# Performance work log

Measured on AMD Instinct MI355X. Metric: run time of the kernel, lower is better.

## Reference

```python
import jax, jax.numpy as jnp
import numpy as np

B, T, N = 8, 4096, 1024
N_KNOWN = 768  # known (sampled) nodes; unknown = N - N_KNOWN = 256
DENSITY = 0.03


def setup_inputs() -> dict:
    key = jax.random.key(0)
    k1, k2, k3, k4 = jax.random.split(key, 4)
    x = jax.random.normal(k1, (B, T, N), dtype=jnp.float32)
    # binary adjacency with ~DENSITY edges; add identity so every node has >=1 neighbor
    A = (jax.random.uniform(k2, (N, N)) < DENSITY).astype(jnp.float32)
    A = jnp.maximum(A, jnp.eye(N, dtype=jnp.float32))
    # unknown = complement(sample, N): 256 distinct node ids, ascending (set-iteration order)
    perm = jax.random.permutation(k3, N)
    unknown = jnp.sort(perm[N_KNOWN:]).astype(jnp.int32)
    # mask = scalar mean of matrix.values[:, sample] in the original module
    mask = jax.random.uniform(k4, (), dtype=jnp.float32)
    return {"input": x, "A": A, "unknown": unknown, "mask": mask}


def reference(input, A, unknown, mask):
    # 1) overwrite unknown columns with the scalar mask (in-place in the original)
    x = input.at[:, :, unknown].set(mask)
    deg = jnp.sum(A, axis=1)  # [N] neighbor counts (A is binary)
    # 2) sequential in-place per-node neighbor mean: later unknown nodes see
    #    the already-updated values of earlier ones, so order matters -> lax.scan.
    def step(x, node):
        # mean over neighbors == masked weighted sum via the binary adjacency row
        val = jnp.einsum('btn,n->bt', x, A[node]) / deg[node]  # [B, T]
        return x.at[:, :, node].set(val), None
    x, _ = jax.lax.scan(step, x, unknown)
    return x
```

## Files before the change

kernel.cpp:

```cpp
#include <hip/hip_runtime.h>

#define U 256
#define NN 1024
#define NROWS 32768
#define LCAP 32
#define DUMMY 256

typedef __bf16 bf16_t;
typedef __bf16 bf16x4 __attribute__((ext_vector_type(4)));
typedef __bf16 bf16x8 __attribute__((ext_vector_type(8)));
typedef float f32x4 __attribute__((ext_vector_type(4)));
typedef unsigned short u16;
typedef unsigned short u16x8 __attribute__((ext_vector_type(8)));
typedef short s16x4 __attribute__((ext_vector_type(4)));

__global__ __launch_bounds__(256) void k_struct(const float* __restrict__ A,
    const int* __restrict__ unknown, const float* __restrict__ maskp,
    float* __restrict__ invDeg, float* __restrict__ coef,
    int* __restrict__ lessCnt, u16* __restrict__ lessIdx,
    int* __restrict__ uflag, short* __restrict__ pmap)
{
    __shared__ int sunk[U];
    __shared__ float sdeg;
    __shared__ int scnt, sge;
    int t = threadIdx.x, k = blockIdx.x;
    sunk[t] = unknown[t];
    if (t == 0) { sdeg = 0.f; scnt = 0; sge = 0; }
    __syncthreads();
    int uk = sunk[k];
    float dsum = 0.f;
    for (int i = 0; i < NN / 256; ++i) {
        int n = t + 256 * i;
        float a = A[(size_t)uk * NN + n];
        if (a != 0.f) {
            dsum += a;
            int lo = 0, hi = U;
            while (lo < hi) { int mid = (lo + hi) >> 1; if (sunk[mid] < n) lo = mid + 1; else hi = mid; }
            if (lo < U && sunk[lo] == n) {
                if (lo < k) {
                    int id = atomicAdd(&scnt, 1);
                    if (id < LCAP) lessIdx[k * LCAP + id] = (u16)lo;
                } else {
                    atomicAdd(&sge, 1);
                }
            }
        }
    }
    atomicAdd(&sdeg, dsum);
    __syncthreads();
    int c0 = min(scnt, LCAP);
    if (t >= c0 && t < LCAP) lessIdx[k * LCAP + t] = DUMMY;
    if (t == 0) {
        float inv = 1.f / sdeg;
        invDeg[k] = inv;
        coef[k] = (float)sge * maskp[0] * inv;
        lessCnt[k] = c0;
    }
    if (k == 0) {
        for (int i = 0; i < NN / 256; ++i) { uflag[t + 256 * i] = 0; pmap[t + 256 * i] = -1; }
        __syncthreads();
        uflag[sunk[t]] = 1;
        pmap[sunk[t]] = (short)t;
    }
}

__global__ __launch_bounds__(256) void k_levels(const int* __restrict__ lessCnt,
    const u16* __restrict__ lessIdx, int* __restrict__ order,
    int* __restrict__ levelStart, int* __restrict__ nLevOut)
{
    __shared__ u16 sIdx[U * LCAP];
    __shared__ int slvl[U];
    __shared__ int sc[U];
    __shared__ int hist[U];
    __shared__ int changed;
    int t = threadIdx.x;
    for (int i = t; i < U * LCAP / 2; i += 256) ((unsigned int*)sIdx)[i] = ((const unsigned int*)lessIdx)[i];
    sc[t] = lessCnt[t];
    slvl[t] = 0; hist[t] = 0;
    __syncthreads();
    for (int iter = 0; iter < U; ++iter) {
        if (t == 0) changed = 0;
        __syncthreads();
        int c = sc[t], nl = 0;
        for (int i = 0; i < c; ++i) nl = max(nl, slvl[sIdx[t * LCAP + i]] + 1);
        if (nl > slvl[t]) { slvl[t] = nl; changed = 1; }
        __syncthreads();
        if (!changed) break;
    }
    int L = slvl[t];
    atomicAdd(&hist[L], 1);
    __syncthreads();
    if (t == 0) {
        int acc = 0, lastl = 0;
        for (int l = 0; l < U; ++l) {
            int h = hist[l];
            hist[l] = acc;
            acc += h;
            if (h > 0) lastl = l;
        }
        nLevOut[0] = lastl + 1;
    }
    __syncthreads();
    levelStart[t] = hist[t];
    if (t == 0) levelStart[U] = U;
    __syncthreads();
    int pos = atomicAdd(&hist[L], 1);
    order[pos] = t;
}

__global__ __launch_bounds__(256) void k_mbuild(const int* __restrict__ lessCnt,
    const u16* __restrict__ lessIdx, const float* __restrict__ invDeg,
    const int* __restrict__ order, const int* __restrict__ levelStart,
    const int* __restrict__ nLevp, float* __restrict__ MT)
{
    __shared__ float Ms[(U + 1) * 32];
    __shared__ u16 sIdx[U * LCAP];
    __shared__ float sInv[U];
    __shared__ u16 sOrd[U];
    __shared__ unsigned char sCnt[U];
    __shared__ int sLs[U + 1];
    int t = threadIdx.x;
    int g = t >> 5, c = t & 31;
    int col = blockIdx.x * 32 + c;
    for (int i = t; i < U * LCAP / 2; i += 256) ((unsigned int*)sIdx)[i] = ((const unsigned int*)lessIdx)[i];
    sInv[t] = invDeg[t];
    sOrd[t] = (u16)order[t];
    sCnt[t] = (unsigned char)lessCnt[t];
    sLs[t] = levelStart[t];
    if (t == 0) sLs[U] = levelStart[U];
    if (t < 32) Ms[U * 32 + t] = 0.f;
    int nLev = nLevp[0];
    __syncthreads();
    for (int lev = 0; lev < nLev; ++lev) {
        int s = sLs[lev], e = sLs[lev + 1];
        for (int base = s + g; base < e; base += 8) {
            int k = sOrd[base];
            int cnt = sCnt[k];
            const u16* ip = &sIdx[k * LCAP];
            float sum = 0.f;
            for (int b = 0; b < cnt; b += 8) {
                u16x8 jv = *(const u16x8*)(ip + b);
                float v0 = Ms[jv[0] * 32 + c];
                float v1 = Ms[jv[1] * 32 + c];
                float v2 = Ms[jv[2] * 32 + c];
                float v3 = Ms[jv[3] * 32 + c];
                float v4 = Ms[jv[4] * 32 + c];
                float v5 = Ms[jv[5] * 32 + c];
                float v6 = Ms[jv[6] * 32 + c];
                float v7 = Ms[jv[7] * 32 + c];
                sum += ((v0 + v1) + (v2 + v3)) + ((v4 + v5) + (v6 + v7));
            }
            float m = (k == col ? 1.f : 0.f) + sInv[k] * sum;
            Ms[k * 32 + c] = m;
            MT[(size_t)col * U + k] = m;
        }
        __syncthreads();
    }
}

__global__ __launch_bounds__(256) void k_wbuild(const float* __restrict__ A,
    const int* __restrict__ unknown, const float* __restrict__ invDeg,
    const float* __restrict__ coef, const int* __restrict__ uflag,
    const float* __restrict__ MT, bf16_t* __restrict__ Wb, float* __restrict__ bvec)
{
    int t = threadIdx.x, d = blockIdx.x;
    if (d == NN) {
        __shared__ float scf[U];
        scf[t] = coef[t];
        __syncthreads();
        float s = 0.f;
        #pragma unroll 8
        for (int c = 0; c < U; ++c) s += MT[(size_t)c * U + t] * scf[c];
        bvec[t] = s;
        return;
    }
    if (uflag[d]) { Wb[(size_t)t * NN + d] = (bf16_t)0.f; return; }
    __shared__ int nnz;
    __shared__ int cs[64];
    __shared__ float vsv[64];
    if (t == 0) nnz = 0;
    __syncthreads();
    float a = A[(size_t)unknown[t] * NN + d];
    if (a != 0.f) {
        int id = atomicAdd(&nnz, 1);
        if (id < 64) { cs[id] = t; vsv[id] = a * invDeg[t]; }
    }
    __syncthreads();
    int n = min(nnz, 64);
    float s = 0.f;
    for (int i = 0; i < n; ++i)
        s += MT[(size_t)cs[i] * U + t] * vsv[i];
    Wb[(size_t)t * NN + d] = (bf16_t)s;
}

#define RT 32
#define BK 64
#define LDX 72
#define URS 257

__global__ __launch_bounds__(256) void k_main(const float* __restrict__ x,
    const short* __restrict__ pmap, const bf16_t* __restrict__ Wb,
    const float* __restrict__ bvec, float* __restrict__ out)
{
    __shared__ __align__(16) char smem[41472];
    __shared__ float sb[U];
    __shared__ short spm[NN];
    bf16_t* Xl = (bf16_t*)smem;
    bf16_t* Vl = (bf16_t*)(smem + 4608);
    float* Ures = (float*)smem;
    int t = threadIdx.x;
    int w = t >> 6, l = t & 63;
    int m = l & 15, q = l >> 4;
    size_t row0 = (size_t)blockIdx.x * RT;
    sb[t] = bvec[t];
    #pragma unroll
    for (int j = 0; j < 4; ++j) spm[t + 256 * j] = pmap[t + 256 * j];
    f32x4 acc[2][4] = {};
    int uv = t >> 3, du = (t & 7) * 8;
    for (int db = 0; db < NN; db += BK) {
        __syncthreads();
        #pragma unroll
        for (int ii = 0; ii < 2; ++ii) {
            int flat = t + ii * 256;
            int r = flat >> 4, c4 = (flat & 15) * 4;
            float4 v = *(const float4*)(x + (row0 + r) * NN + db + c4);
            bf16x4 hv = { (bf16_t)v.x, (bf16_t)v.y, (bf16_t)v.z, (bf16_t)v.w };
            *(bf16x4*)(&Xl[r * LDX + c4]) = hv;
        }
        #pragma unroll
        for (int i = 0; i < 8; ++i) {
            int u = uv + 32 * i;
            *(bf16x8*)(&Vl[u * LDX + du]) = *(const bf16x8*)(Wb + (size_t)u * NN + db + du);
        }
        __syncthreads();
        #pragma unroll
        for (int s = 0; s < 2; ++s) {
            bf16x8 af[2];
            #pragma unroll
            for (int R = 0; R < 2; ++R)
                af[R] = *(bf16x8*)(&Xl[(R * 16 + m) * LDX + s * 32 + q * 8]);
            #pragma unroll
            for (int T = 0; T < 4; ++T) {
                bf16x8 bfr = *(bf16x8*)(&Vl[((w * 4 + T) * 16 + m) * LDX + s * 32 + q * 8]);
                #pragma unroll
                for (int R = 0; R < 2; ++R)
                    acc[R][T] = __builtin_amdgcn_mfma_f32_16x16x32_bf16(af[R], bfr, acc[R][T], 0, 0, 0);
            }
        }
    }
    __syncthreads();
    #pragma unroll
    for (int R = 0; R < 2; ++R) {
        #pragma unroll
        for (int T = 0; T < 4; ++T) {
            int u = (w * 4 + T) * 16 + m;
            float bb = sb[u];
            #pragma unroll
            for (int i = 0; i < 4; ++i)
                Ures[(R * 16 + q * 4 + i) * URS + u] = acc[R][T][i] + bb;
        }
    }
    __syncthreads();
    s16x4 pm = *(const s16x4*)(&spm[t * 4]);
    #pragma unroll 4
    for (int i = 0; i < RT; ++i) {
        float4 v = *(const float4*)(x + (row0 + i) * NN + t * 4);
        if (pm[0] >= 0) v.x = Ures[i * URS + pm[0]];
        if (pm[1] >= 0) v.y = Ures[i * URS + pm[1]];
        if (pm[2] >= 0) v.z = Ures[i * URS + pm[2]];
        if (pm[3] >= 0) v.w = Ures[i * URS + pm[3]];
        *(float4*)(out + (row0 + i) * NN + t * 4) = v;
    }
}

extern "C" void kernel_launch(void* const* d_in, const int* in_sizes, int n_in,
                              void* d_out, int out_size, void* d_ws, size_t ws_size,
                              hipStream_t stream)
{
    const float* x       = (const float*)d_in[0];
    const float* A       = (const float*)d_in[1];
    const int*   unknown = (const int*)d_in[2];
    const float* maskp   = (const float*)d_in[3];
    float* out = (float*)d_out;

    char* ws = (char*)d_ws;
    float*  MT        = (float*)(ws + 0);
    bf16_t* Wb        = (bf16_t*)(ws + 262144);
    float*  invDeg    = (float*)(ws + 786432);
    float*  coef      = (float*)(ws + 787456);
    float*  bvec      = (float*)(ws + 788480);
    int*    lessCnt   = (int*)(ws + 789504);
    u16*    lessIdx   = (u16*)(ws + 790528);
    int*    uflag     = (int*)(ws + 806912);
    short*  pmap      = (short*)(ws + 811008);
    int*    order     = (int*)(ws + 813056);
    int*    levelStart= (int*)(ws + 814080);
    int*    nLev      = (int*)(ws + 815120);

    hipLaunchKernelGGL(k_struct, dim3(U), dim3(256), 0, stream,
                       A, unknown, maskp, invDeg, coef, lessCnt, lessIdx, uflag, pmap);
    hipLaunchKernelGGL(k_levels, dim3(1), dim3(256), 0, stream,
                       lessCnt, lessIdx, order, levelStart, nLev);
    hipLaunchKernelGGL(k_mbuild, dim3(8), dim3(256), 0, stream,
                       lessCnt, lessIdx, invDeg, order, levelStart, nLev, MT);
    hipLaunchKernelGGL(k_wbuild, dim3(NN + 1), dim3(256), 0, stream,
                       A, unknown, invDeg, coef, uflag, MT, Wb, bvec);
    hipLaunchKernelGGL(k_main, dim3(NROWS / RT), dim3(256), 0, stream,
                       x, pmap, Wb, bvec, out);
}
```

Before: 348.2 us.

## Double the row tile and prefetch next K-chunk into registers

The main GEMM kernel now processes 64 rows per block instead of 32, so each Wb tile loaded into LDS is reused across twice as many rows. Global loads for the next K-chunk are issued into registers before the MFMA work on the current chunk, so load latency overlaps compute. The epilogue writes results in two halves to fit the existing Ures buffer, and launch bounds ask for two blocks per CU. Costs are more registers per thread and half as many blocks (512), which may reduce occupancy and parallelism.

```diff
diff --git a/kernel.cpp b/kernel.cpp
--- a/kernel.cpp
+++ b/kernel.cpp
@@ -193,20 +193,20 @@
     Wb[(size_t)t * NN + d] = (bf16_t)s;
 }
 
-#define RT 32
+#define RT 64
 #define BK 64
 #define LDX 72
 #define URS 257
 
-__global__ __launch_bounds__(256) void k_main(const float* __restrict__ x,
+__global__ __launch_bounds__(256, 2) void k_main(const float* __restrict__ x,
     const short* __restrict__ pmap, const bf16_t* __restrict__ Wb,
     const float* __restrict__ bvec, float* __restrict__ out)
 {
-    __shared__ __align__(16) char smem[41472];
+    __shared__ __align__(16) char smem[46080];
     __shared__ float sb[U];
     __shared__ short spm[NN];
     bf16_t* Xl = (bf16_t*)smem;
-    bf16_t* Vl = (bf16_t*)(smem + 4608);
+    bf16_t* Vl = (bf16_t*)(smem + 9216);
     float* Ures = (float*)smem;
     int t = threadIdx.x;
     int w = t >> 6, l = t & 63;
@@ -215,61 +215,82 @@
     sb[t] = bvec[t];
     #pragma unroll
     for (int j = 0; j < 4; ++j) spm[t + 256 * j] = pmap[t + 256 * j];
-    f32x4 acc[2][4] = {};
+    f32x4 acc[4][4] = {};
     int uv = t >> 3, du = (t & 7) * 8;
+
+    float4 xr[4];
+    bf16x8 vr[8];
+
+#define LOADC(DB) do { \
+    _Pragma("unroll") \
+    for (int ii = 0; ii < 4; ++ii) { \
+        int flat = t + ii * 256; \
+        int r = flat >> 4, c4 = (flat & 15) * 4; \
+        xr[ii] = *(const float4*)(x + (row0 + r) * NN + (DB) + c4); \
+    } \
+    _Pragma("unroll") \
+    for (int i = 0; i < 8; ++i) \
+        vr[i] = *(const bf16x8*)(Wb + (size_t)(uv + 32 * i) * NN + (DB) + du); \
+} while (0)
+
+    LOADC(0);
     for (int db = 0; db < NN; db += BK) {
         __syncthreads();
         #pragma unroll
-        for (int ii = 0; ii < 2; ++ii) {
+        for (int ii = 0; ii < 4; ++ii) {
             int flat = t + ii * 256;
             int r = flat >> 4, c4 = (flat & 15) * 4;
-            float4 v = *(const float4*)(x + (row0 + r) * NN + db + c4);
+            float4 v = xr[ii];
             bf16x4 hv = { (bf16_t)v.x, (bf16_t)v.y, (bf16_t)v.z, (bf16_t)v.w };
             *(bf16x4*)(&Xl[r * LDX + c4]) = hv;
         }
         #pragma unroll
-        for (int i = 0; i < 8; ++i) {
-            int u = uv + 32 * i;
-            *(bf16x8*)(&Vl[u * LDX + du]) = *(const bf16x8*)(Wb + (size_t)u * NN + db + du);
-        }
-        __syncthreads();
+        for (int i = 0; i < 8; ++i)
+            *(bf16x8*)(&Vl[(uv + 32 * i) * LDX + du]) = vr[i];
+        __syncthreads();
+        if (db + BK < NN) LOADC(db + BK);
         #pragma unroll
         for (int s = 0; s < 2; ++s) {
-            bf16x8 af[2];
+            bf16x8 af[4];
             #pragma unroll
-            for (int R = 0; R < 2; ++R)
+            for (int R = 0; R < 4; ++R)
                 af[R] = *(bf16x8*)(&Xl[(R * 16 + m) * LDX + s * 32 + q * 8]);
             #pragma unroll
             for (int T = 0; T < 4; ++T) {
                 bf16x8 bfr = *(bf16x8*)(&Vl[((w * 4 + T) * 16 + m) * LDX + s * 32 + q * 8]);
                 #pragma unroll
-                for (int R = 0; R < 2; ++R)
+                for (int R = 0; R < 4; ++R)
                     acc[R][T] = __builtin_amdgcn_mfma_f32_16x16x32_bf16(af[R], bfr, acc[R][T], 0, 0, 0);
             }
         }
     }
-    __syncthreads();
+#undef LOADC
     #pragma unroll
-    for (int R = 0; R < 2; ++R) {
+    for (int h = 0; h < 2; ++h) {
+        __syncthreads();
         #pragma unroll
-        for (int T = 0; T < 4; ++T) {
-            int u = (w * 4 + T) * 16 + m;
-            float bb = sb[u];
+        for (int R2 = 0; R2 < 2; ++R2) {
+            int R = 2 * h + R2;
             #pragma unroll
-            for (int i = 0; i < 4; ++i)
-                Ures[(R * 16 + q * 4 + i) * URS + u] = acc[R][T][i] + bb;
-        }
-    }
-    __syncthreads();
-    s16x4 pm = *(const s16x4*)(&spm[t * 4]);
-    #pragma unroll 4
-    for (int i = 0; i < RT; ++i) {
-        float4 v = *(const float4*)(x + (row0 + i) * NN + t * 4);
-        if (pm[0] >= 0) v.x = Ures[i * URS + pm[0]];
-        if (pm[1] >= 0) v.y = Ures[i * URS + pm[1]];
-        if (pm[2] >= 0) v.z = Ures[i * URS + pm[2]];
-        if (pm[3] >= 0) v.w = Ures[i * URS + pm[3]];
-        *(float4*)(out + (row0 + i) * NN + t * 4) = v;
+            for (int T = 0; T < 4; ++T) {
+                int u = (w * 4 + T) * 16 + m;
+                float bb = sb[u];
+                #pragma unroll
+                for (int i = 0; i < 4; ++i)
+                    Ures[(R2 * 16 + q * 4 + i) * URS + u] = acc[R][T][i] + bb;
+            }
+        }
+        __syncthreads();
+        s16x4 pm = *(const s16x4*)(&spm[t * 4]);
+        #pragma unroll 4
+        for (int i = 0; i < 32; ++i) {
+            float4 v = *(const float4*)(x + (row0 + h * 32 + i) * NN + t * 4);
+            if (pm[0] >= 0) v.x = Ures[i * URS + pm[0]];
+            if (pm[1] >= 0) v.y = Ures[i * URS + pm[1]];
+            if (pm[2] >= 0) v.z = Ures[i * URS + pm[2]];
+            if (pm[3] >= 0) v.w = Ures[i * URS + pm[3]];
+            *(float4*)(out + (row0 + h * 32 + i) * NN + t * 4) = v;
+        }
     }
 }
 
```

Result: faster. 323.4 us (-7.1%).

## Fuse setup kernels into one cooperative launch and prefetch next tile in main GEMM

Applied to the files above, without the earlier changes.

Merges the four preprocessing kernels (structure, levels, M build, W build) into a single cooperative kernel separated by grid syncs, removing three launch gaps. The W build now has 256 blocks each handling four columns. The main kernel register-prefetches the next x and W tile before the MFMA loop to overlap global loads with compute, and raises launch bounds to target three blocks per CU. The cooperative launch needs all 256 blocks to be co-resident, and the extra prefetch registers may raise register pressure.

```diff
diff --git a/kernel.cpp b/kernel.cpp
--- a/kernel.cpp
+++ b/kernel.cpp
@@ -1,4 +1,7 @@
 #include <hip/hip_runtime.h>
+#include <hip/hip_cooperative_groups.h>
+
+namespace cg = cooperative_groups;
 
 #define U 256
 #define NN 1024
@@ -14,183 +17,193 @@
 typedef unsigned short u16x8 __attribute__((ext_vector_type(8)));
 typedef short s16x4 __attribute__((ext_vector_type(4)));
 
-__global__ __launch_bounds__(256) void k_struct(const float* __restrict__ A,
+__global__ __launch_bounds__(256) void k_setup(const float* __restrict__ A,
     const int* __restrict__ unknown, const float* __restrict__ maskp,
     float* __restrict__ invDeg, float* __restrict__ coef,
     int* __restrict__ lessCnt, u16* __restrict__ lessIdx,
-    int* __restrict__ uflag, short* __restrict__ pmap)
+    int* __restrict__ uflag, short* __restrict__ pmap,
+    int* __restrict__ order, int* __restrict__ levelStart, int* __restrict__ nLev,
+    float* __restrict__ MT, bf16_t* __restrict__ Wb, float* __restrict__ bvec)
 {
+    cg::grid_group grid = cg::this_grid();
     __shared__ int sunk[U];
     __shared__ float sdeg;
     __shared__ int scnt, sge;
-    int t = threadIdx.x, k = blockIdx.x;
-    sunk[t] = unknown[t];
-    if (t == 0) { sdeg = 0.f; scnt = 0; sge = 0; }
-    __syncthreads();
-    int uk = sunk[k];
-    float dsum = 0.f;
-    for (int i = 0; i < NN / 256; ++i) {
-        int n = t + 256 * i;
-        float a = A[(size_t)uk * NN + n];
-        if (a != 0.f) {
-            dsum += a;
-            int lo = 0, hi = U;
-            while (lo < hi) { int mid = (lo + hi) >> 1; if (sunk[mid] < n) lo = mid + 1; else hi = mid; }
-            if (lo < U && sunk[lo] == n) {
-                if (lo < k) {
-                    int id = atomicAdd(&scnt, 1);
-                    if (id < LCAP) lessIdx[k * LCAP + id] = (u16)lo;
-                } else {
-                    atomicAdd(&sge, 1);
-                }
-            }
-        }
-    }
-    atomicAdd(&sdeg, dsum);
-    __syncthreads();
-    int c0 = min(scnt, LCAP);
-    if (t >= c0 && t < LCAP) lessIdx[k * LCAP + t] = DUMMY;
-    if (t == 0) {
-        float inv = 1.f / sdeg;
-        invDeg[k] = inv;
-        coef[k] = (float)sge * maskp[0] * inv;
-        lessCnt[k] = c0;
-    }
-    if (k == 0) {
-        for (int i = 0; i < NN / 256; ++i) { uflag[t + 256 * i] = 0; pmap[t + 256 * i] = -1; }
-        __syncthreads();
-        uflag[sunk[t]] = 1;
-        pmap[sunk[t]] = (short)t;
-    }
-}
-
-__global__ __launch_bounds__(256) void k_levels(const int* __restrict__ lessCnt,
-    const u16* __restrict__ lessIdx, int* __restrict__ order,
-    int* __restrict__ levelStart, int* __restrict__ nLevOut)
-{
     __shared__ u16 sIdx[U * LCAP];
     __shared__ int slvl[U];
-    __shared__ int sc[U];
+    __shared__ int scL[U];
     __shared__ int hist[U];
     __shared__ int changed;
-    int t = threadIdx.x;
-    for (int i = t; i < U * LCAP / 2; i += 256) ((unsigned int*)sIdx)[i] = ((const unsigned int*)lessIdx)[i];
-    sc[t] = lessCnt[t];
-    slvl[t] = 0; hist[t] = 0;
-    __syncthreads();
-    for (int iter = 0; iter < U; ++iter) {
-        if (t == 0) changed = 0;
-        __syncthreads();
-        int c = sc[t], nl = 0;
-        for (int i = 0; i < c; ++i) nl = max(nl, slvl[sIdx[t * LCAP + i]] + 1);
-        if (nl > slvl[t]) { slvl[t] = nl; changed = 1; }
-        __syncthreads();
-        if (!changed) break;
-    }
-    int L = slvl[t];
-    atomicAdd(&hist[L], 1);
-    __syncthreads();
-    if (t == 0) {
-        int acc = 0, lastl = 0;
-        for (int l = 0; l < U; ++l) {
-            int h = hist[l];
-            hist[l] = acc;
-            acc += h;
-            if (h > 0) lastl = l;
-        }
-        nLevOut[0] = lastl + 1;
-    }
-    __syncthreads();
-    levelStart[t] = hist[t];
-    if (t == 0) levelStart[U] = U;
-    __syncthreads();
-    int pos = atomicAdd(&hist[L], 1);
-    order[pos] = t;
-}
-
-__global__ __launch_bounds__(256) void k_mbuild(const int* __restrict__ lessCnt,
-    const u16* __restrict__ lessIdx, const float* __restrict__ invDeg,
-    const int* __restrict__ order, const int* __restrict__ levelStart,
-    const int* __restrict__ nLevp, float* __restrict__ MT)
-{
     __shared__ float Ms[(U + 1) * 32];
-    __shared__ u16 sIdx[U * LCAP];
     __shared__ float sInv[U];
     __shared__ u16 sOrd[U];
     __shared__ unsigned char sCnt[U];
     __shared__ int sLs[U + 1];
-    int t = threadIdx.x;
-    int g = t >> 5, c = t & 31;
-    int col = blockIdx.x * 32 + c;
-    for (int i = t; i < U * LCAP / 2; i += 256) ((unsigned int*)sIdx)[i] = ((const unsigned int*)lessIdx)[i];
-    sInv[t] = invDeg[t];
-    sOrd[t] = (u16)order[t];
-    sCnt[t] = (unsigned char)lessCnt[t];
-    sLs[t] = levelStart[t];
-    if (t == 0) sLs[U] = levelStart[U];
-    if (t < 32) Ms[U * 32 + t] = 0.f;
-    int nLev = nLevp[0];
-    __syncthreads();
-    for (int lev = 0; lev < nLev; ++lev) {
-        int s = sLs[lev], e = sLs[lev + 1];
-        for (int base = s + g; base < e; base += 8) {
-            int k = sOrd[base];
-            int cnt = sCnt[k];
-            const u16* ip = &sIdx[k * LCAP];
-            float sum = 0.f;
-            for (int b = 0; b < cnt; b += 8) {
-                u16x8 jv = *(const u16x8*)(ip + b);
-                float v0 = Ms[jv[0] * 32 + c];
-                float v1 = Ms[jv[1] * 32 + c];
-                float v2 = Ms[jv[2] * 32 + c];
-                float v3 = Ms[jv[3] * 32 + c];
-                float v4 = Ms[jv[4] * 32 + c];
-                float v5 = Ms[jv[5] * 32 + c];
-                float v6 = Ms[jv[6] * 32 + c];
-                float v7 = Ms[jv[7] * 32 + c];
-                sum += ((v0 + v1) + (v2 + v3)) + ((v4 + v5) + (v6 + v7));
-            }
-            float m = (k == col ? 1.f : 0.f) + sInv[k] * sum;
-            Ms[k * 32 + c] = m;
-            MT[(size_t)col * U + k] = m;
-        }
-        __syncthreads();
-    }
-}
-
-__global__ __launch_bounds__(256) void k_wbuild(const float* __restrict__ A,
-    const int* __restrict__ unknown, const float* __restrict__ invDeg,
-    const float* __restrict__ coef, const int* __restrict__ uflag,
-    const float* __restrict__ MT, bf16_t* __restrict__ Wb, float* __restrict__ bvec)
-{
-    int t = threadIdx.x, d = blockIdx.x;
-    if (d == NN) {
-        __shared__ float scf[U];
-        scf[t] = coef[t];
-        __syncthreads();
-        float s = 0.f;
-        #pragma unroll 8
-        for (int c = 0; c < U; ++c) s += MT[(size_t)c * U + t] * scf[c];
-        bvec[t] = s;
-        return;
-    }
-    if (uflag[d]) { Wb[(size_t)t * NN + d] = (bf16_t)0.f; return; }
     __shared__ int nnz;
     __shared__ int cs[64];
     __shared__ float vsv[64];
-    if (t == 0) nnz = 0;
+    __shared__ float scf[U];
+
+    int t = threadIdx.x, k = blockIdx.x;
+
+    sunk[t] = unknown[t];
+    if (t == 0) { sdeg = 0.f; scnt = 0; sge = 0; }
     __syncthreads();
-    float a = A[(size_t)unknown[t] * NN + d];
-    if (a != 0.f) {
-        int id = atomicAdd(&nnz, 1);
-        if (id < 64) { cs[id] = t; vsv[id] = a * invDeg[t]; }
-    }
-    __syncthreads();
-    int n = min(nnz, 64);
-    float s = 0.f;
-    for (int i = 0; i < n; ++i)
-        s += MT[(size_t)cs[i] * U + t] * vsv[i];
-    Wb[(size_t)t * NN + d] = (bf16_t)s;
+    {
+        int uk = sunk[k];
+        float dsum = 0.f;
+        for (int i = 0; i < NN / 256; ++i) {
+            int n = t + 256 * i;
+            float a = A[(size_t)uk * NN + n];
+            if (a != 0.f) {
+                dsum += a;
+                int lo = 0, hi = U;
+                while (lo < hi) { int mid = (lo + hi) >> 1; if (sunk[mid] < n) lo = mid + 1; else hi = mid; }
+                if (lo < U && sunk[lo] == n) {
+                    if (lo < k) {
+                        int id = atomicAdd(&scnt, 1);
+                        if (id < LCAP) lessIdx[k * LCAP + id] = (u16)lo;
+                    } else {
+                        atomicAdd(&sge, 1);
+                    }
+                }
+            }
+        }
+        atomicAdd(&sdeg, dsum);
+        __syncthreads();
+        int c0 = min(scnt, LCAP);
+        if (t >= c0 && t < LCAP) lessIdx[k * LCAP + t] = DUMMY;
+        if (t == 0) {
+            float inv = 1.f / sdeg;
+            invDeg[k] = inv;
+            coef[k] = (float)sge * maskp[0] * inv;
+            lessCnt[k] = c0;
+        }
+        if (k == 0) {
+            for (int i = 0; i < NN / 256; ++i) { uflag[t + 256 * i] = 0; pmap[t + 256 * i] = -1; }
+            __syncthreads();
+            uflag[sunk[t]] = 1;
+            pmap[sunk[t]] = (short)t;
+        }
+    }
+    __threadfence();
+    grid.sync();
+
+    if (k == 0) {
+        for (int i = t; i < U * LCAP / 2; i += 256) ((unsigned int*)sIdx)[i] = ((const unsigned int*)lessIdx)[i];
+        scL[t] = lessCnt[t];
+        slvl[t] = 0; hist[t] = 0;
+        __syncthreads();
+        for (int iter = 0; iter < U; ++iter) {
+            if (t == 0) changed = 0;
+            __syncthreads();
+            int c = scL[t], nl = 0;
+            for (int i = 0; i < c; ++i) nl = max(nl, slvl[sIdx[t * LCAP + i]] + 1);
+            if (nl > slvl[t]) { slvl[t] = nl; changed = 1; }
+            __syncthreads();
+            if (!changed) break;
+        }
+        int L = slvl[t];
+        atomicAdd(&hist[L], 1);
+        __syncthreads();
+        if (t == 0) {
+            int acc = 0, lastl = 0;
+            for (int l = 0; l < U; ++l) {
+                int h = hist[l];
+                hist[l] = acc;
+                acc += h;
+                if (h > 0) lastl = l;
+            }
+            nLev[0] = lastl + 1;
+        }
+        __syncthreads();
+        levelStart[t] = hist[t];
+        if (t == 0) levelStart[U] = U;
+        __syncthreads();
+        int pos = atomicAdd(&hist[L], 1);
+        order[pos] = t;
+    }
+    __threadfence();
+    grid.sync();
+
+    if (k < 8) {
+        int g = t >> 5, c = t & 31;
+        int col = k * 32 + c;
+        for (int i = t; i < U * LCAP / 2; i += 256) ((unsigned int*)sIdx)[i] = ((const unsigned int*)lessIdx)[i];
+        sInv[t] = invDeg[t];
+        sOrd[t] = (u16)order[t];
+        sCnt[t] = (unsigned char)lessCnt[t];
+        sLs[t] = levelStart[t];
+        if (t == 0) sLs[U] = levelStart[U];
+        if (t < 32) Ms[U * 32 + t] = 0.f;
+        int nlv = nLev[0];
+        __syncthreads();
+        for (int lev = 0; lev < nlv; ++lev) {
+            int s = sLs[lev], e = sLs[lev + 1];
+            for (int base = s + g; base < e; base += 8) {
+                int nd = sOrd[base];
+                int cnt = sCnt[nd];
+                const u16* ip = &sIdx[nd * LCAP];
+                float sum = 0.f;
+                for (int b = 0; b < cnt; b += 8) {
+                    u16x8 jv = *(const u16x8*)(ip + b);
+                    float v0 = Ms[jv[0] * 32 + c];
+                    float v1 = Ms[jv[1] * 32 + c];
+                    float v2 = Ms[jv[2] * 32 + c];
+                    float v3 = Ms[jv[3] * 32 + c];
+                    float v4 = Ms[jv[4] * 32 + c];
+                    float v5 = Ms[jv[5] * 32 + c];
+                    float v6 = Ms[jv[6] * 32 + c];
+                    float v7 = Ms[jv[7] * 32 + c];
+                    sum += ((v0 + v1) + (v2 + v3)) + ((v4 + v5) + (v6 + v7));
+                }
+                float m = (nd == col ? 1.f : 0.f) + sInv[nd] * sum;
+                Ms[nd * 32 + c] = m;
+                MT[(size_t)col * U + nd] = m;
+            }
+            __syncthreads();
+        }
+    }
+    __threadfence();
+    grid.sync();
+
+    {
+        int unk = sunk[t];
+        float inv = invDeg[t];
+        for (int dd = 0; dd < 4; ++dd) {
+            int d = k + 256 * dd;
+            __syncthreads();
+            if (t == 0) nnz = 0;
+            __syncthreads();
+            int skip = uflag[d];
+            if (!skip) {
+                float a = A[(size_t)unk * NN + d];
+                if (a != 0.f) {
+                    int id = atomicAdd(&nnz, 1);
+                    if (id < 64) { cs[id] = t; vsv[id] = a * inv; }
+                }
+            }
+            __syncthreads();
+            if (skip) {
+                Wb[(size_t)t * NN + d] = (bf16_t)0.f;
+            } else {
+                int n = min(nnz, 64);
+                float s = 0.f;
+                for (int i = 0; i < n; ++i)
+                    s += MT[(size_t)cs[i] * U + t] * vsv[i];
+                Wb[(size_t)t * NN + d] = (bf16_t)s;
+            }
+        }
+        if (k == 0) {
+            __syncthreads();
+            scf[t] = coef[t];
+            __syncthreads();
+            float s = 0.f;
+            #pragma unroll 8
+            for (int c = 0; c < U; ++c) s += MT[(size_t)c * U + t] * scf[c];
+            bvec[t] = s;
+        }
+    }
 }
 
 #define RT 32
@@ -198,7 +211,7 @@
 #define LDX 72
 #define URS 257
 
-__global__ __launch_bounds__(256) void k_main(const float* __restrict__ x,
+__global__ __launch_bounds__(256, 3) void k_main(const float* __restrict__ x,
     const short* __restrict__ pmap, const bf16_t* __restrict__ Wb,
     const float* __restrict__ bvec, float* __restrict__ out)
 {
@@ -217,22 +230,38 @@
     for (int j = 0; j < 4; ++j) spm[t + 256 * j] = pmap[t + 256 * j];
     f32x4 acc[2][4] = {};
     int uv = t >> 3, du = (t & 7) * 8;
+
+    float4 xr[2];
+    bf16x8 vr[8];
+
+#define LOADC(DB) do { \
+    _Pragma("unroll") \
+    for (int ii = 0; ii < 2; ++ii) { \
+        int flat = t + ii * 256; \
+        int r = flat >> 4, c4 = (flat & 15) * 4; \
+        xr[ii] = *(const float4*)(x + (row0 + r) * NN + (DB) + c4); \
+    } \
+    _Pragma("unroll") \
+    for (int i = 0; i < 8; ++i) \
+        vr[i] = *(const bf16x8*)(Wb + (size_t)(uv + 32 * i) * NN + (DB) + du); \
+} while (0)
+
+    LOADC(0);
     for (int db = 0; db < NN; db += BK) {
         __syncthreads();
         #pragma unroll
         for (int ii = 0; ii < 2; ++ii) {
             int flat = t + ii * 256;
             int r = flat >> 4, c4 = (flat & 15) * 4;
-            float4 v = *(const float4*)(x + (row0 + r) * NN + db + c4);
+            float4 v = xr[ii];
             bf16x4 hv = { (bf16_t)v.x, (bf16_t)v.y, (bf16_t)v.z, (bf16_t)v.w };
             *(bf16x4*)(&Xl[r * LDX + c4]) = hv;
         }
         #pragma unroll
-        for (int i = 0; i < 8; ++i) {
-            int u = uv + 32 * i;
-            *(bf16x8*)(&Vl[u * LDX + du]) = *(const bf16x8*)(Wb + (size_t)u * NN + db + du);
-        }
-        __syncthreads();
+        for (int i = 0; i < 8; ++i)
+            *(bf16x8*)(&Vl[(uv + 32 * i) * LDX + du]) = vr[i];
+        __syncthreads();
+        if (db + BK < NN) LOADC(db + BK);
         #pragma unroll
         for (int s = 0; s < 2; ++s) {
             bf16x8 af[2];
@@ -248,6 +277,7 @@
             }
         }
     }
+#undef LOADC
     __syncthreads();
     #pragma unroll
     for (int R = 0; R < 2; ++R) {
@@ -297,14 +327,12 @@
     int*    levelStart= (int*)(ws + 814080);
     int*    nLev      = (int*)(ws + 815120);
 
-    hipLaunchKernelGGL(k_struct, dim3(U), dim3(256), 0, stream,
-                       A, unknown, maskp, invDeg, coef, lessCnt, lessIdx, uflag, pmap);
-    hipLaunchKernelGGL(k_levels, dim3(1), dim3(256), 0, stream,
-                       lessCnt, lessIdx, order, levelStart, nLev);
-    hipLaunchKernelGGL(k_mbuild, dim3(8), dim3(256), 0, stream,
-                       lessCnt, lessIdx, invDeg, order, levelStart, nLev, MT);
-    hipLaunchKernelGGL(k_wbuild, dim3(NN + 1), dim3(256), 0, stream,
-                       A, unknown, invDeg, coef, uflag, MT, Wb, bvec);
+    void* cargs[15] = { (void*)&A, (void*)&unknown, (void*)&maskp, (void*)&invDeg,
+                        (void*)&coef, (void*)&lessCnt, (void*)&lessIdx, (void*)&uflag,
+                        (void*)&pmap, (void*)&order, (void*)&levelStart, (void*)&nLev,
+                        (void*)&MT, (void*)&Wb, (void*)&bvec };
+    hipLaunchCooperativeKernel((void*)k_setup, dim3(U), dim3(256), cargs, 0, stream);
+
     hipLaunchKernelGGL(k_main, dim3(NROWS / RT), dim3(256), 0, stream,
                        x, pmap, Wb, bvec, out);
 }
```

New measurement: 474.5 us. 1.36x slower.

## Merge level scheduling into M build, register-prefetch main GEMM with 64-row tiles

Applied to the files above, without the earlier changes.

Folds the single-block level computation into k_mbuild, so each of the 8 blocks recomputes levels redundantly instead of paying a separate launch. The bias vector is now accumulated atomically at the end of k_mbuild rather than in an extra k_wbuild block. k_main moves to 512-thread blocks covering 64 rows and prefetches the next K-tile of x and Wb into registers while the MFMAs run, so Wb staging is amortised over twice as many rows. The cost is higher register pressure and a two-phase epilogue that adds extra barriers, plus atomic float adds for bvec that make its summation order nondeterministic.

```diff
diff --git a/kernel.cpp b/kernel.cpp
--- a/kernel.cpp
+++ b/kernel.cpp
@@ -18,7 +18,7 @@
     const int* __restrict__ unknown, const float* __restrict__ maskp,
     float* __restrict__ invDeg, float* __restrict__ coef,
     int* __restrict__ lessCnt, u16* __restrict__ lessIdx,
-    int* __restrict__ uflag, short* __restrict__ pmap)
+    int* __restrict__ uflag, short* __restrict__ pmap, float* __restrict__ bvec)
 {
     __shared__ int sunk[U];
     __shared__ float sdeg;
@@ -58,31 +58,41 @@
     }
     if (k == 0) {
         for (int i = 0; i < NN / 256; ++i) { uflag[t + 256 * i] = 0; pmap[t + 256 * i] = -1; }
+        bvec[t] = 0.f;
         __syncthreads();
         uflag[sunk[t]] = 1;
         pmap[sunk[t]] = (short)t;
     }
 }
 
-__global__ __launch_bounds__(256) void k_levels(const int* __restrict__ lessCnt,
-    const u16* __restrict__ lessIdx, int* __restrict__ order,
-    int* __restrict__ levelStart, int* __restrict__ nLevOut)
+__global__ __launch_bounds__(256) void k_mbuild(const int* __restrict__ lessCnt,
+    const u16* __restrict__ lessIdx, const float* __restrict__ invDeg,
+    const float* __restrict__ coef, float* __restrict__ MT, float* __restrict__ bvec)
 {
     __shared__ u16 sIdx[U * LCAP];
     __shared__ int slvl[U];
-    __shared__ int sc[U];
     __shared__ int hist[U];
     __shared__ int changed;
+    __shared__ int snl;
+    __shared__ float Ms[(U + 1) * 32];
+    __shared__ float sInv[U];
+    __shared__ u16 sOrd[U];
+    __shared__ unsigned char sCnt[U];
+    __shared__ int sLs[U + 1];
+    __shared__ float scf[U];
     int t = threadIdx.x;
     for (int i = t; i < U * LCAP / 2; i += 256) ((unsigned int*)sIdx)[i] = ((const unsigned int*)lessIdx)[i];
-    sc[t] = lessCnt[t];
+    int myCnt = lessCnt[t];
+    sCnt[t] = (unsigned char)myCnt;
+    sInv[t] = invDeg[t];
+    scf[t] = coef[t];
     slvl[t] = 0; hist[t] = 0;
     __syncthreads();
     for (int iter = 0; iter < U; ++iter) {
         if (t == 0) changed = 0;
         __syncthreads();
-        int c = sc[t], nl = 0;
-        for (int i = 0; i < c; ++i) nl = max(nl, slvl[sIdx[t * LCAP + i]] + 1);
+        int nl = 0;
+        for (int i = 0; i < myCnt; ++i) nl = max(nl, slvl[sIdx[t * LCAP + i]] + 1);
         if (nl > slvl[t]) { slvl[t] = nl; changed = 1; }
         __syncthreads();
         if (!changed) break;
@@ -98,40 +108,20 @@
             acc += h;
             if (h > 0) lastl = l;
         }
-        nLevOut[0] = lastl + 1;
-    }
-    __syncthreads();
-    levelStart[t] = hist[t];
-    if (t == 0) levelStart[U] = U;
+        snl = lastl + 1;
+    }
+    __syncthreads();
+    sLs[t] = hist[t];
+    if (t == 0) sLs[U] = U;
+    if (t < 32) Ms[U * 32 + t] = 0.f;
     __syncthreads();
     int pos = atomicAdd(&hist[L], 1);
-    order[pos] = t;
-}
-
-__global__ __launch_bounds__(256) void k_mbuild(const int* __restrict__ lessCnt,
-    const u16* __restrict__ lessIdx, const float* __restrict__ invDeg,
-    const int* __restrict__ order, const int* __restrict__ levelStart,
-    const int* __restrict__ nLevp, float* __restrict__ MT)
-{
-    __shared__ float Ms[(U + 1) * 32];
-    __shared__ u16 sIdx[U * LCAP];
-    __shared__ float sInv[U];
-    __shared__ u16 sOrd[U];
-    __shared__ unsigned char sCnt[U];
-    __shared__ int sLs[U + 1];
-    int t = threadIdx.x;
+    sOrd[pos] = (u16)t;
+    int nlv = snl;
+    __syncthreads();
     int g = t >> 5, c = t & 31;
     int col = blockIdx.x * 32 + c;
-    for (int i = t; i < U * LCAP / 2; i += 256) ((unsigned int*)sIdx)[i] = ((const unsigned int*)lessIdx)[i];
-    sInv[t] = invDeg[t];
-    sOrd[t] = (u16)order[t];
-    sCnt[t] = (unsigned char)lessCnt[t];
-    sLs[t] = levelStart[t];
-    if (t == 0) sLs[U] = levelStart[U];
-    if (t < 32) Ms[U * 32 + t] = 0.f;
-    int nLev = nLevp[0];
-    __syncthreads();
-    for (int lev = 0; lev < nLev; ++lev) {
+    for (int lev = 0; lev < nlv; ++lev) {
         int s = sLs[lev], e = sLs[lev + 1];
         for (int base = s + g; base < e; base += 8) {
             int k = sOrd[base];
@@ -156,24 +146,21 @@
         }
         __syncthreads();
     }
+    float s = 0.f;
+    #pragma unroll 8
+    for (int j = 0; j < 32; ++j) {
+        int cl = (j + (t & 31)) & 31;
+        s += Ms[t * 32 + cl] * scf[blockIdx.x * 32 + cl];
+    }
+    atomicAdd(&bvec[t], s);
 }
 
 __global__ __launch_bounds__(256) void k_wbuild(const float* __restrict__ A,
     const int* __restrict__ unknown, const float* __restrict__ invDeg,
-    const float* __restrict__ coef, const int* __restrict__ uflag,
-    const float* __restrict__ MT, bf16_t* __restrict__ Wb, float* __restrict__ bvec)
+    const int* __restrict__ uflag, const float* __restrict__ MT,
+    bf16_t* __restrict__ Wb)
 {
     int t = threadIdx.x, d = blockIdx.x;
-    if (d == NN) {
-        __shared__ float scf[U];
-        scf[t] = coef[t];
-        __syncthreads();
-        float s = 0.f;
-        #pragma unroll 8
-        for (int c = 0; c < U; ++c) s += MT[(size_t)c * U + t] * scf[c];
-        bvec[t] = s;
-        return;
-    }
     if (uflag[d]) { Wb[(size_t)t * NN + d] = (bf16_t)0.f; return; }
     __shared__ int nnz;
     __shared__ int cs[64];
@@ -193,83 +180,108 @@
     Wb[(size_t)t * NN + d] = (bf16_t)s;
 }
 
-#define RT 32
+#define RT 64
 #define BK 64
 #define LDX 72
 #define URS 257
 
-__global__ __launch_bounds__(256) void k_main(const float* __restrict__ x,
+__global__ __launch_bounds__(512, 4) void k_main(const float* __restrict__ x,
     const short* __restrict__ pmap, const bf16_t* __restrict__ Wb,
     const float* __restrict__ bvec, float* __restrict__ out)
 {
-    __shared__ __align__(16) char smem[41472];
+    __shared__ __align__(16) char smem[46080];
     __shared__ float sb[U];
     __shared__ short spm[NN];
     bf16_t* Xl = (bf16_t*)smem;
-    bf16_t* Vl = (bf16_t*)(smem + 4608);
+    bf16_t* Vl = (bf16_t*)(smem + 9216);
     float* Ures = (float*)smem;
     int t = threadIdx.x;
     int w = t >> 6, l = t & 63;
     int m = l & 15, q = l >> 4;
+    int rg = w >> 2, cg = w & 3;
     size_t row0 = (size_t)blockIdx.x * RT;
-    sb[t] = bvec[t];
-    #pragma unroll
-    for (int j = 0; j < 4; ++j) spm[t + 256 * j] = pmap[t + 256 * j];
+    if (t < U) sb[t] = bvec[t];
+    spm[t] = pmap[t];
+    spm[t + 512] = pmap[t + 512];
     f32x4 acc[2][4] = {};
     int uv = t >> 3, du = (t & 7) * 8;
+
+    float4 xr[2];
+    bf16x8 vr[4];
+
+#define LOADC(DB) do { \
+    _Pragma("unroll") \
+    for (int ii = 0; ii < 2; ++ii) { \
+        int flat = t + ii * 512; \
+        int r = flat >> 4, c4 = (flat & 15) * 4; \
+        xr[ii] = *(const float4*)(x + (row0 + r) * NN + (DB) + c4); \
+    } \
+    _Pragma("unroll") \
+    for (int i = 0; i < 4; ++i) \
+        vr[i] = *(const bf16x8*)(Wb + (size_t)(uv + 64 * i) * NN + (DB) + du); \
+} while (0)
+
+    LOADC(0);
     for (int db = 0; db < NN; db += BK) {
         __syncthreads();
         #pragma unroll
         for (int ii = 0; ii < 2; ++ii) {
-            int flat = t + ii * 256;
+            int flat = t + ii * 512;
             int r = flat >> 4, c4 = (flat & 15) * 4;
-            float4 v = *(const float4*)(x + (row0 + r) * NN + db + c4);
+            float4 v = xr[ii];
             bf16x4 hv = { (bf16_t)v.x, (bf16_t)v.y, (bf16_t)v.z, (bf16_t)v.w };
             *(bf16x4*)(&Xl[r * LDX + c4]) = hv;
         }
         #pragma unroll
-        for (int i = 0; i < 8; ++i) {
-            int u = uv + 32 * i;
-            *(bf16x8*)(&Vl[u * LDX + du]) = *(const bf16x8*)(Wb + (size_t)u * NN + db + du);
-        }
-        __syncthreads();
+        for (int i = 0; i < 4; ++i)
+            *(bf16x8*)(&Vl[(uv + 64 * i) * LDX + du]) = vr[i];
+        __syncthreads();
+        if (db + BK < NN) LOADC(db + BK);
         #pragma unroll
         for (int s = 0; s < 2; ++s) {
             bf16x8 af[2];
             #pragma unroll
             for (int R = 0; R < 2; ++R)
-                af[R] = *(bf16x8*)(&Xl[(R * 16 + m) * LDX + s * 32 + q * 8]);
+                af[R] = *(bf16x8*)(&Xl[(rg * 32 + R * 16 + m) * LDX + s * 32 + q * 8]);
             #pragma unroll
             for (int T = 0; T < 4; ++T) {
-                bf16x8 bfr = *(bf16x8*)(&Vl[((w * 4 + T) * 16 + m) * LDX + s * 32 + q * 8]);
+                bf16x8 bfr = *(bf16x8*)(&Vl[((cg * 4 + T) * 16 + m) * LDX + s * 32 + q * 8]);
                 #pragma unroll
                 for (int R = 0; R < 2; ++R)
                     acc[R][T] = __builtin_amdgcn_mfma_f32_16x16x32_bf16(af[R], bfr, acc[R][T], 0, 0, 0);
             }
         }
     }
-    __syncthreads();
+#undef LOADC
     #pragma unroll
-    for (int R = 0; R < 2; ++R) {
-        #pragma unroll
-        for (int T = 0; T < 4; ++T) {
-            int u = (w * 4 + T) * 16 + m;
-            float bb = sb[u];
+    for (int h = 0; h < 2; ++h) {
+        __syncthreads();
+        if (rg == h) {
             #pragma unroll
-            for (int i = 0; i < 4; ++i)
-                Ures[(R * 16 + q * 4 + i) * URS + u] = acc[R][T][i] + bb;
-        }
-    }
-    __syncthreads();
-    s16x4 pm = *(const s16x4*)(&spm[t * 4]);
-    #pragma unroll 4
-    for (int i = 0; i < RT; ++i) {
-        float4 v = *(const float4*)(x + (row0 + i) * NN + t * 4);
-        if (pm[0] >= 0) v.x = Ures[i * URS + pm[0]];
-        if (pm[1] >= 0) v.y = Ures[i * URS + pm[1]];
-        if (pm[2] >= 0) v.z = Ures[i * URS + pm[2]];
-        if (pm[3] >= 0) v.w = Ures[i * URS + pm[3]];
-        *(float4*)(out + (row0 + i) * NN + t * 4) = v;
+            for (int R = 0; R < 2; ++R) {
+                #pragma unroll
+                for (int T = 0; T < 4; ++T) {
+                    int u = (cg * 4 + T) * 16 + m;
+                    float bb = sb[u];
+                    #pragma unroll
+                    for (int i = 0; i < 4; ++i)
+                        Ures[(R * 16 + q * 4 + i) * URS + u] = acc[R][T][i] + bb;
+                }
+            }
+        }
+        __syncthreads();
+        int c4i = t & 255, rh = t >> 8;
+        s16x4 pm = *(const s16x4*)(&spm[c4i * 4]);
+        #pragma unroll 4
+        for (int it = 0; it < 16; ++it) {
+            int lr = 2 * it + rh;
+            float4 v = *(const float4*)(x + (row0 + h * 32 + lr) * NN + c4i * 4);
+            if (pm[0] >= 0) v.x = Ures[lr * URS + pm[0]];
+            if (pm[1] >= 0) v.y = Ures[lr * URS + pm[1]];
+            if (pm[2] >= 0) v.z = Ures[lr * URS + pm[2]];
+            if (pm[3] >= 0) v.w = Ures[lr * URS + pm[3]];
+            *(float4*)(out + (row0 + h * 32 + lr) * NN + c4i * 4) = v;
+        }
     }
 }
 
@@ -284,27 +296,22 @@
     float* out = (float*)d_out;
 
     char* ws = (char*)d_ws;
-    float*  MT        = (float*)(ws + 0);
-    bf16_t* Wb        = (bf16_t*)(ws + 262144);
-    float*  invDeg    = (float*)(ws + 786432);
-    float*  coef      = (float*)(ws + 787456);
-    float*  bvec      = (float*)(ws + 788480);
-    int*    lessCnt   = (int*)(ws + 789504);
-    u16*    lessIdx   = (u16*)(ws + 790528);
-    int*    uflag     = (int*)(ws + 806912);
-    short*  pmap      = (short*)(ws + 811008);
-    int*    order     = (int*)(ws + 813056);
-    int*    levelStart= (int*)(ws + 814080);
-    int*    nLev      = (int*)(ws + 815120);
+    float*  MT      = (float*)(ws + 0);
+    bf16_t* Wb      = (bf16_t*)(ws + 262144);
+    float*  invDeg  = (float*)(ws + 786432);
+    float*  coef    = (float*)(ws + 787456);
+    float*  bvec    = (float*)(ws + 788480);
+    int*    lessCnt = (int*)(ws + 789504);
+    u16*    lessIdx = (u16*)(ws + 790528);
+    int*    uflag   = (int*)(ws + 806912);
+    short*  pmap    = (short*)(ws + 811008);
 
     hipLaunchKernelGGL(k_struct, dim3(U), dim3(256), 0, stream,
-                       A, unknown, maskp, invDeg, coef, lessCnt, lessIdx, uflag, pmap);
-    hipLaunchKernelGGL(k_levels, dim3(1), dim3(256), 0, stream,
-                       lessCnt, lessIdx, order, levelStart, nLev);
+                       A, unknown, maskp, invDeg, coef, lessCnt, lessIdx, uflag, pmap, bvec);
     hipLaunchKernelGGL(k_mbuild, dim3(8), dim3(256), 0, stream,
-                       lessCnt, lessIdx, invDeg, order, levelStart, nLev, MT);
-    hipLaunchKernelGGL(k_wbuild, dim3(NN + 1), dim3(256), 0, stream,
-                       A, unknown, invDeg, coef, uflag, MT, Wb, bvec);
-    hipLaunchKernelGGL(k_main, dim3(NROWS / RT), dim3(256), 0, stream,
+                       lessCnt, lessIdx, invDeg, coef, MT, bvec);
+    hipLaunchKernelGGL(k_wbuild, dim3(NN), dim3(256), 0, stream,
+                       A, unknown, invDeg, uflag, MT, Wb);
+    hipLaunchKernelGGL(k_main, dim3(NROWS / RT), dim3(512), 0, stream,
                        x, pmap, Wb, bvec, out);
 }
```

After: 314.3 us. 9.7% less time.
